# Kernel optimization log

Hardware: AMD Instinct MI355X
Metric: run time of the kernel (lower is better)

The kernel has to match this reference:

```python
import jax, jax.numpy as jnp
import numpy as np

NEG_SLOPE = 0.2
EPS = 1e-16  # PyG softmax denominator epsilon


def gatv2_layer(x, src, dst, W_l, W_r, att, bias, num_nodes, heads, out_dim, concat):
    # x: [N, F_in]; src/dst: [E] (self-loops already included)
    x_l = (x @ W_l).reshape(num_nodes, heads, out_dim)  # source transform
    x_r = (x @ W_r).reshape(num_nodes, heads, out_dim)  # target transform
    # GATv2 scoring: a^T LeakyReLU(x_l[j] + x_r[i])
    e = jax.nn.leaky_relu(x_l[src] + x_r[dst], NEG_SLOPE)       # [E, H, D]
    logits = jnp.einsum('ehd,hd->eh', e, att)                    # [E, H]
    # segment softmax over incoming edges of each target node
    m = jax.ops.segment_max(logits, dst, num_segments=num_nodes)  # [N, H]
    ex = jnp.exp(logits - m[dst])                                 # [E, H]
    denom = jax.ops.segment_sum(ex, dst, num_segments=num_nodes)  # [N, H]
    alpha = ex / (denom[dst] + EPS)                               # [E, H]
    msg = x_l[src] * alpha[:, :, None]                            # [E, H, D]
    out = jax.ops.segment_sum(msg, dst, num_segments=num_nodes)   # [N, H, D]
    if concat:
        out = out.reshape(num_nodes, heads * out_dim)
    else:
        out = out.mean(axis=1)
    return out + bias


def setup_inputs() -> dict:
    key = jax.random.key(0)
    ks = jax.random.split(key, 10)
    N, E, F_in, H, D, F_out = 50000, 400000, 256, 4, 128, 64

    def glorot(k, shape, fan):
        return jax.random.normal(k, shape, dtype=jnp.float32) * (1.0 / np.sqrt(fan))

    return {
        'x': jax.random.normal(ks[0], (N, F_in), dtype=jnp.float32),
        'edge_index': jax.random.randint(ks[1], (2, E), 0, N, dtype=jnp.int64),
        'W_l1': glorot(ks[2], (F_in, H * D), F_in),
        'W_r1': glorot(ks[3], (F_in, H * D), F_in),
        'att1': glorot(ks[4], (H, D), D),
        'b1': jnp.zeros((H * D,), dtype=jnp.float32),
        'W_l2': glorot(ks[5], (H * D, F_out), H * D),
        'W_r2': glorot(ks[6], (H * D, F_out), H * D),
        'att2': glorot(ks[7], (1, F_out), F_out),
        'b2': jnp.zeros((F_out,), dtype=jnp.float32),
    }


def reference(x, edge_index, W_l1, W_r1, att1, b1, W_l2, W_r2, att2, b2):
    N = x.shape[0]
    # add self-loops (PyG GATv2Conv default add_self_loops=True)
    loops = jnp.arange(N, dtype=edge_index.dtype)
    src = jnp.concatenate([edge_index[0], loops])
    dst = jnp.concatenate([edge_index[1], loops])
    # dropout(p=0.6) is identity in eval mode
    h = gatv2_layer(x, src, dst, W_l1, W_r1, att1, b1, N, heads=4, out_dim=128, concat=True)
    h = jax.nn.elu(h)
    out = gatv2_layer(h, src, dst, W_l2, W_r2, att2, b2, N, heads=1, out_dim=64, concat=False)
    return out
```

## Files before the change

kernel.cpp:

```cpp
#include <hip/hip_runtime.h>
#include <hip/hip_bf16.h>
#include <math.h>


#define NEG_SLOPE 0.2f

typedef _Float16 half8 __attribute__((ext_vector_type(8)));
typedef float f32x4 __attribute__((ext_vector_type(4)));

struct __align__(4) h2f { _Float16 x, y; };


__global__ __launch_bounds__(256) void k_zero(int* __restrict__ p, int n) {
    int i = blockIdx.x * 256 + threadIdx.x;
    if (i < n) p[i] = 0;
}

__global__ __launch_bounds__(256) void k_count(const int* __restrict__ ei, int* __restrict__ counts,
                                               int E, int Etot) {
    int i = blockIdx.x * 256 + threadIdx.x;
    if (i >= Etot) return;
    int dst = (i < E) ? ei[E + i] : (i - E);
    atomicAdd(&counts[dst], 1);
}

__global__ __launch_bounds__(1024) void k_scan_a(const int* __restrict__ counts, int* __restrict__ offs,
                                                 int* __restrict__ partial, int n) {
    __shared__ int buf[1024];
    int b = blockIdx.x, t = threadIdx.x;
    int i = b * 1024 + t;
    int v = (i < n) ? counts[i] : 0;
    buf[t] = v;
    __syncthreads();
    #pragma unroll
    for (int off = 1; off < 1024; off <<= 1) {
        int add = (t >= off) ? buf[t - off] : 0;
        __syncthreads();
        buf[t] += add;
        __syncthreads();
    }
    if (i < n) offs[i + 1] = buf[t];
    if (t == 1023) partial[b] = buf[1023];
}

__global__ __launch_bounds__(1024) void k_scan_b(int* __restrict__ partial, int nb) {
    __shared__ int buf[1024];
    int t = threadIdx.x;
    int v = (t < nb) ? partial[t] : 0;
    buf[t] = v;
    __syncthreads();
    #pragma unroll
    for (int off = 1; off < 1024; off <<= 1) {
        int add = (t >= off) ? buf[t - off] : 0;
        __syncthreads();
        buf[t] += add;
        __syncthreads();
    }
    if (t < nb) partial[t] = buf[t] - v;
}

__global__ __launch_bounds__(256) void k_scan_c(int* __restrict__ offs, int* __restrict__ cursor,
                                                const int* __restrict__ partial, int n) {
    int i = blockIdx.x * 256 + threadIdx.x;
    if (i == 0) { offs[0] = 0; cursor[0] = 0; }
    if (i < n) {
        int v = offs[i + 1] + partial[i >> 10];
        offs[i + 1] = v;
        cursor[i + 1] = v;
    }
}

__global__ __launch_bounds__(256) void k_fill(const int* __restrict__ ei, int* __restrict__ cursor,
                                              int* __restrict__ csr_src, int E, int Etot) {
    int i = blockIdx.x * 256 + threadIdx.x;
    if (i >= Etot) return;
    int src, dst;
    if (i < E) { src = ei[i]; dst = ei[E + i]; }
    else       { src = i - E; dst = i - E; }
    int pos = atomicAdd(&cursor[dst], 1);
    csr_src[pos] = src;
}


__global__ __launch_bounds__(256) void k_cast_x(const float* __restrict__ in, _Float16* __restrict__ out,
                                                int n8) {
    int i = blockIdx.x * 256 + threadIdx.x;
    if (i >= n8) return;
    const float4* p = (const float4*)(in + i * 8);
    float4 a = p[0], b = p[1];
    half8 v;
    v[0] = (_Float16)a.x; v[1] = (_Float16)a.y; v[2] = (_Float16)a.z; v[3] = (_Float16)a.w;
    v[4] = (_Float16)b.x; v[5] = (_Float16)b.y; v[6] = (_Float16)b.z; v[7] = (_Float16)b.w;
    *(half8*)(out + i * 8) = v;
}

__global__ __launch_bounds__(256) void k_cast_wcat(const float* __restrict__ Wa, const float* __restrict__ Wb,
                                                   _Float16* __restrict__ out, int K, int Nh) {
    int i = blockIdx.x * 256 + threadIdx.x;
    int total = 2 * Nh * K;
    if (i >= total) return;
    int n = i / K, k = i - n * K;
    float v = (n < Nh) ? Wa[k * Nh + n] : Wb[k * Nh + (n - Nh)];
    out[i] = (_Float16)v;
}


#define LDSPITCH 40

__global__ __launch_bounds__(256) void k_gemm_f16(const _Float16* __restrict__ A,
                                                  const _Float16* __restrict__ Bt,
                                                  _Float16* __restrict__ C,
                                                  int M, int N, int K) {
    __shared__ _Float16 As[128 * LDSPITCH];
    __shared__ _Float16 Bs[128 * LDSPITCH];

    int tid = threadIdx.x;
    int lane = tid & 63;
    int wave = tid >> 6;
    int wm = wave >> 1, wn = wave & 1;
    int l15 = lane & 15, q = lane >> 4;

    int tileM = blockIdx.x * 128;
    int tileN = blockIdx.y * 128;

    int srow = tid >> 2;
    int scg  = (tid & 3) * 8;

    f32x4 acc[4][4];
    #pragma unroll
    for (int i = 0; i < 4; ++i)
        #pragma unroll
        for (int j = 0; j < 4; ++j)
            acc[i][j] = (f32x4)(0.f);

    for (int k0 = 0; k0 < K; k0 += 32) {
        float4 va0, va1, vb0, vb1;
        {
            int r0 = tileM + srow, r1 = tileM + srow + 64;
            const float4 z = make_float4(0.f, 0.f, 0.f, 0.f);
            va0 = (r0 < M) ? *(const float4*)(A + (long)r0 * K + k0 + scg) : z;
            va1 = (r1 < M) ? *(const float4*)(A + (long)r1 * K + k0 + scg) : z;
            vb0 = *(const float4*)(Bt + (long)(tileN + srow) * K + k0 + scg);
            vb1 = *(const float4*)(Bt + (long)(tileN + srow + 64) * K + k0 + scg);
        }
        __syncthreads();
        *(float4*)(As + srow * LDSPITCH + scg) = va0;
        *(float4*)(As + (srow + 64) * LDSPITCH + scg) = va1;
        *(float4*)(Bs + srow * LDSPITCH + scg) = vb0;
        *(float4*)(Bs + (srow + 64) * LDSPITCH + scg) = vb1;
        __syncthreads();

        half8 af[4], bf[4];
        #pragma unroll
        for (int i = 0; i < 4; ++i)
            af[i] = *(half8*)(As + (wm * 64 + i * 16 + l15) * LDSPITCH + q * 8);
        #pragma unroll
        for (int j = 0; j < 4; ++j)
            bf[j] = *(half8*)(Bs + (wn * 64 + j * 16 + l15) * LDSPITCH + q * 8);
        #pragma unroll
        for (int i = 0; i < 4; ++i)
            #pragma unroll
            for (int j = 0; j < 4; ++j)
                acc[i][j] = __builtin_amdgcn_mfma_f32_16x16x32_f16(af[i], bf[j], acc[i][j], 0, 0, 0);
    }

    #pragma unroll
    for (int i = 0; i < 4; ++i) {
        #pragma unroll
        for (int r = 0; r < 4; ++r) {
            int grow = tileM + wm * 64 + i * 16 + q * 4 + r;
            if (grow < M) {
                #pragma unroll
                for (int j = 0; j < 4; ++j) {
                    int gcol = tileN + wn * 64 + j * 16 + l15;
                    C[(long)grow * N + gcol] = (_Float16)acc[i][j][r];
                }
            }
        }
    }
}


__global__ __launch_bounds__(256) void k_attn1(const _Float16* __restrict__ xlr,
                                               const float* __restrict__ att, const float* __restrict__ b1,
                                               const int* __restrict__ offs, const int* __restrict__ csr_src,
                                               _Float16* __restrict__ hout, int N) {
    int wave = threadIdx.x >> 6;
    int lane = threadIdx.x & 63;
    int node = blockIdx.x * 4 + wave;
    if (node >= N) return;

    int cbase = (lane >> 4) * 128 + (lane & 15) * 8;

    half8 xrv = *(const half8*)(xlr + (long)node * 1024 + 512 + cbase);
    float xr[8], at[8];
    #pragma unroll
    for (int j = 0; j < 8; ++j) { xr[j] = (float)xrv[j]; at[j] = att[cbase + j]; }

    float l = 0.f;
    float acc[8] = {};

    int e0 = offs[node], e1 = offs[node + 1];
    int src = csr_src[e0];
    half8 xlv = *(const half8*)(xlr + (long)src * 1024 + cbase);

    for (int e = e0; e < e1; ++e) {
        half8 cur = xlv;
        if (e + 1 < e1) {
            int s2 = csr_src[e + 1];
            xlv = *(const half8*)(xlr + (long)s2 * 1024 + cbase);
        }
        float xf[8];
        float p = 0.f;
        #pragma unroll
        for (int j = 0; j < 8; ++j) {
            xf[j] = (float)cur[j];
            float t = xf[j] + xr[j];
            t = fmaxf(t, NEG_SLOPE * t);
            p = fmaf(t, at[j], p);
        }
        #pragma unroll
        for (int off = 1; off <= 8; off <<= 1) p += __shfl_xor(p, off, 64);
        float w = __expf(p);
        l += w;
        #pragma unroll
        for (int j = 0; j < 8; ++j) acc[j] = fmaf(w, xf[j], acc[j]);
    }

    float inv = 1.f / (l + 1e-16f);
    half8 ov;
    #pragma unroll
    for (int j = 0; j < 8; ++j) {
        float o = fmaf(acc[j], inv, b1[cbase + j]);
        o = (o > 0.f) ? o : (__expf(o) - 1.f);
        ov[j] = (_Float16)o;
    }
    *(half8*)(hout + (long)node * 512 + cbase) = ov;
}


__global__ __launch_bounds__(256) void k_attn2(const _Float16* __restrict__ xlr2,
                                               const float* __restrict__ att, const float* __restrict__ b2,
                                               const int* __restrict__ offs, const int* __restrict__ csr_src,
                                               float* __restrict__ out, int N) {
    int wave = threadIdx.x >> 6;
    int lane = threadIdx.x & 63;
    int node = blockIdx.x * 4 + wave;
    if (node >= N) return;

    float xrv = (float)xlr2[(long)node * 128 + 64 + lane];
    float av  = att[lane];

    float l = 0.f, acc = 0.f;
    int e0 = offs[node], e1 = offs[node + 1];
    int src = csr_src[e0];
    float xlv = (float)xlr2[(long)src * 128 + lane];

    for (int e = e0; e < e1; ++e) {
        float x = xlv;
        if (e + 1 < e1) {
            int s2 = csr_src[e + 1];
            xlv = (float)xlr2[(long)s2 * 128 + lane];
        }
        float t = x + xrv;
        t = fmaxf(t, NEG_SLOPE * t);
        float p = t * av;
        #pragma unroll
        for (int off = 1; off <= 32; off <<= 1) p += __shfl_xor(p, off, 64);
        float w = __expf(p);
        l += w;
        acc = fmaf(w, x, acc);
    }
    out[(long)node * 64 + lane] = acc / (l + 1e-16f) + b2[lane];
}


extern "C" void kernel_launch(void* const* d_in, const int* in_sizes, int n_in,
                              void* d_out, int out_size, void* d_ws, size_t ws_size,
                              hipStream_t stream) {
    const float* x    = (const float*)d_in[0];
    const int*   ei   = (const int*)d_in[1];
    const float* Wl1  = (const float*)d_in[2];
    const float* Wr1  = (const float*)d_in[3];
    const float* att1 = (const float*)d_in[4];
    const float* b1   = (const float*)d_in[5];
    const float* Wl2  = (const float*)d_in[6];
    const float* Wr2  = (const float*)d_in[7];
    const float* att2 = (const float*)d_in[8];
    const float* b2   = (const float*)d_in[9];
    float* out = (float*)d_out;

    const int F_IN = 256;
    int N = in_sizes[0] / F_IN;
    int E = in_sizes[1] / 2;
    int Etot = E + N;
    int nScanBlocks = (N + 1023) / 1024;

    char* p = (char*)d_ws;
    auto carve = [&](size_t bytes) -> void* {
        void* r = (void*)p;
        p += (bytes + 255) & ~(size_t)255;
        return r;
    };
    _Float16* xh   = (_Float16*)carve((size_t)N * 256 * 2);
    _Float16* W1T  = (_Float16*)carve((size_t)1024 * 256 * 2);
    _Float16* W2T  = (_Float16*)carve((size_t)128 * 512 * 2);
    _Float16* C1   = (_Float16*)carve((size_t)N * 1024 * 2);
    _Float16* h    = (_Float16*)carve((size_t)N * 512 * 2);
    _Float16* C2   = (_Float16*)carve((size_t)N * 128 * 2);
    int* counts  = (int*)carve((size_t)N * 4);
    int* offs    = (int*)carve((size_t)(N + 1) * 4);
    int* cursor  = (int*)carve((size_t)(N + 1) * 4);
    int* partial = (int*)carve((size_t)nScanBlocks * 4);
    int* csr     = (int*)carve((size_t)Etot * 4);

    int gN    = (N + 255) / 256;
    int gEtot = (Etot + 255) / 256;

    k_cast_x<<<(N * 256 / 8 + 255) / 256, 256, 0, stream>>>(x, xh, N * 256 / 8);
    k_cast_wcat<<<(1024 * 256 + 255) / 256, 256, 0, stream>>>(Wl1, Wr1, W1T, 256, 512);
    k_cast_wcat<<<(128 * 512 + 255) / 256, 256, 0, stream>>>(Wl2, Wr2, W2T, 512, 64);

    k_zero<<<gN, 256, 0, stream>>>(counts, N);
    k_count<<<gEtot, 256, 0, stream>>>(ei, counts, E, Etot);
    k_scan_a<<<nScanBlocks, 1024, 0, stream>>>(counts, offs, partial, N);
    k_scan_b<<<1, 1024, 0, stream>>>(partial, nScanBlocks);
    k_scan_c<<<gN, 256, 0, stream>>>(offs, cursor, partial, N);
    k_fill<<<gEtot, 256, 0, stream>>>(ei, cursor, csr, E, Etot);

    {
        dim3 grid((N + 127) / 128, 1024 / 128);
        k_gemm_f16<<<grid, 256, 0, stream>>>(xh, W1T, C1, N, 1024, 256);
    }
    k_attn1<<<(N + 3) / 4, 256, 0, stream>>>(C1, att1, b1, offs, csr, h, N);

    {
        dim3 grid((N + 127) / 128, 1);
        k_gemm_f16<<<grid, 256, 0, stream>>>(h, W2T, C2, N, 128, 512);
    }
    k_attn2<<<(N + 3) / 4, 256, 0, stream>>>(C2, att2, b2, offs, csr, out, N);
}
```

Baseline: 389.9 us.

## Use packed fp16 dot2 scoring, deeper index prefetch, fused weight casts, N-major GEMM grid

Layer-1 attention scoring now runs on packed half2 math with an fdot2 accumulate instead of per-element fp32 converts and FMAs. Both attention kernels prefetch the source index two edges ahead so the index load no longer sits on the gather path. The two weight-cast kernels are merged into one launch, the zeroing kernel is replaced with hipMemsetAsync, and the GEMM grid is linearised so the N tiles that share an M tile run back to back. fp16 LeakyReLU and logit accumulation lose some precision compared with fp32.

```diff
diff --git a/kernel.cpp b/kernel.cpp
--- a/kernel.cpp
+++ b/kernel.cpp
@@ -6,15 +6,9 @@
 #define NEG_SLOPE 0.2f
 
 typedef _Float16 half8 __attribute__((ext_vector_type(8)));
+typedef _Float16 h2 __attribute__((ext_vector_type(2)));
 typedef float f32x4 __attribute__((ext_vector_type(4)));
 
-struct __align__(4) h2f { _Float16 x, y; };
-
-
-__global__ __launch_bounds__(256) void k_zero(int* __restrict__ p, int n) {
-    int i = blockIdx.x * 256 + threadIdx.x;
-    if (i < n) p[i] = 0;
-}
 
 __global__ __launch_bounds__(256) void k_count(const int* __restrict__ ei, int* __restrict__ counts,
                                                int E, int Etot) {
@@ -94,14 +88,22 @@
     *(half8*)(out + i * 8) = v;
 }
 
-__global__ __launch_bounds__(256) void k_cast_wcat(const float* __restrict__ Wa, const float* __restrict__ Wb,
-                                                   _Float16* __restrict__ out, int K, int Nh) {
-    int i = blockIdx.x * 256 + threadIdx.x;
-    int total = 2 * Nh * K;
-    if (i >= total) return;
-    int n = i / K, k = i - n * K;
-    float v = (n < Nh) ? Wa[k * Nh + n] : Wb[k * Nh + (n - Nh)];
-    out[i] = (_Float16)v;
+__global__ __launch_bounds__(256) void k_cast_w(const float* __restrict__ Wl1, const float* __restrict__ Wr1,
+                                                const float* __restrict__ Wl2, const float* __restrict__ Wr2,
+                                                _Float16* __restrict__ W1T, _Float16* __restrict__ W2T) {
+    int i = blockIdx.x * 256 + threadIdx.x;
+    const int T1 = 1024 * 256;
+    const int T2 = 128 * 512;
+    if (i < T1) {
+        int n = i >> 8, k = i & 255;
+        float v = (n < 512) ? Wl1[k * 512 + n] : Wr1[k * 512 + (n - 512)];
+        W1T[i] = (_Float16)v;
+    } else if (i < T1 + T2) {
+        int j = i - T1;
+        int n = j >> 9, k = j & 511;
+        float v = (n < 64) ? Wl2[k * 64 + n] : Wr2[k * 64 + (n - 64)];
+        W2T[j] = (_Float16)v;
+    }
 }
 
 
@@ -110,7 +112,7 @@
 __global__ __launch_bounds__(256) void k_gemm_f16(const _Float16* __restrict__ A,
                                                   const _Float16* __restrict__ Bt,
                                                   _Float16* __restrict__ C,
-                                                  int M, int N, int K) {
+                                                  int M, int N, int K, int ntiles) {
     __shared__ _Float16 As[128 * LDSPITCH];
     __shared__ _Float16 Bs[128 * LDSPITCH];
 
@@ -120,8 +122,10 @@
     int wm = wave >> 1, wn = wave & 1;
     int l15 = lane & 15, q = lane >> 4;
 
-    int tileM = blockIdx.x * 128;
-    int tileN = blockIdx.y * 128;
+    int ntile = blockIdx.x % ntiles;
+    int mtile = blockIdx.x / ntiles;
+    int tileM = mtile * 128;
+    int tileN = ntile * 128;
 
     int srow = tid >> 2;
     int scg  = (tid & 3) * 8;
@@ -181,6 +185,14 @@
 }
 
 
+__device__ __forceinline__ float dot2acc(h2 a, h2 b, float c) {
+#if __has_builtin(__builtin_amdgcn_fdot2)
+    return __builtin_amdgcn_fdot2(a, b, c, false);
+#else
+    return fmaf((float)a[1], (float)b[1], fmaf((float)a[0], (float)b[0], c));
+#endif
+}
+
 __global__ __launch_bounds__(256) void k_attn1(const _Float16* __restrict__ xlr,
                                                const float* __restrict__ att, const float* __restrict__ b1,
                                                const int* __restrict__ offs, const int* __restrict__ csr_src,
@@ -192,39 +204,50 @@
 
     int cbase = (lane >> 4) * 128 + (lane & 15) * 8;
 
-    half8 xrv = *(const half8*)(xlr + (long)node * 1024 + 512 + cbase);
-    float xr[8], at[8];
-    #pragma unroll
-    for (int j = 0; j < 8; ++j) { xr[j] = (float)xrv[j]; at[j] = att[cbase + j]; }
+    half8 xrv8 = *(const half8*)(xlr + (long)node * 1024 + 512 + cbase);
+    h2 xr[4], at[4];
+    #pragma unroll
+    for (int j = 0; j < 4; ++j) {
+        xr[j][0] = xrv8[2 * j]; xr[j][1] = xrv8[2 * j + 1];
+        at[j][0] = (_Float16)att[cbase + 2 * j];
+        at[j][1] = (_Float16)att[cbase + 2 * j + 1];
+    }
+    const h2 ns2 = {(_Float16)NEG_SLOPE, (_Float16)NEG_SLOPE};
 
     float l = 0.f;
     float acc[8] = {};
 
     int e0 = offs[node], e1 = offs[node + 1];
-    int src = csr_src[e0];
-    half8 xlv = *(const half8*)(xlr + (long)src * 1024 + cbase);
+    int s_next = csr_src[e0];
+    int s_next2 = (e0 + 1 < e1) ? csr_src[e0 + 1] : 0;
+    half8 xlv = *(const half8*)(xlr + (long)s_next * 1024 + cbase);
 
     for (int e = e0; e < e1; ++e) {
         half8 cur = xlv;
-        if (e + 1 < e1) {
-            int s2 = csr_src[e + 1];
-            xlv = *(const half8*)(xlr + (long)s2 * 1024 + cbase);
-        }
-        float xf[8];
+        int s_pf = s_next2;
+        if (e + 2 < e1) s_next2 = csr_src[e + 2];
+        if (e + 1 < e1) xlv = *(const half8*)(xlr + (long)s_pf * 1024 + cbase);
+
+        const h2* cp = (const h2*)&cur;
         float p = 0.f;
         #pragma unroll
-        for (int j = 0; j < 8; ++j) {
-            xf[j] = (float)cur[j];
-            float t = xf[j] + xr[j];
-            t = fmaxf(t, NEG_SLOPE * t);
-            p = fmaf(t, at[j], p);
+        for (int j = 0; j < 4; ++j) {
+            h2 t = cp[j] + xr[j];
+#if __has_builtin(__builtin_elementwise_max)
+            t = __builtin_elementwise_max(t, t * ns2);
+#else
+            h2 tn = t * ns2;
+            t[0] = (t[0] > tn[0]) ? t[0] : tn[0];
+            t[1] = (t[1] > tn[1]) ? t[1] : tn[1];
+#endif
+            p = dot2acc(t, at[j], p);
         }
         #pragma unroll
         for (int off = 1; off <= 8; off <<= 1) p += __shfl_xor(p, off, 64);
         float w = __expf(p);
         l += w;
         #pragma unroll
-        for (int j = 0; j < 8; ++j) acc[j] = fmaf(w, xf[j], acc[j]);
+        for (int j = 0; j < 8; ++j) acc[j] = fmaf(w, (float)cur[j], acc[j]);
     }
 
     float inv = 1.f / (l + 1e-16f);
@@ -253,15 +276,16 @@
 
     float l = 0.f, acc = 0.f;
     int e0 = offs[node], e1 = offs[node + 1];
-    int src = csr_src[e0];
-    float xlv = (float)xlr2[(long)src * 128 + lane];
+    int s_next = csr_src[e0];
+    int s_next2 = (e0 + 1 < e1) ? csr_src[e0 + 1] : 0;
+    float xlv = (float)xlr2[(long)s_next * 128 + lane];
 
     for (int e = e0; e < e1; ++e) {
         float x = xlv;
-        if (e + 1 < e1) {
-            int s2 = csr_src[e + 1];
-            xlv = (float)xlr2[(long)s2 * 128 + lane];
-        }
+        int s_pf = s_next2;
+        if (e + 2 < e1) s_next2 = csr_src[e + 2];
+        if (e + 1 < e1) xlv = (float)xlr2[(long)s_pf * 128 + lane];
+
         float t = x + xrv;
         t = fmaxf(t, NEG_SLOPE * t);
         float p = t * av;
@@ -318,10 +342,12 @@
     int gEtot = (Etot + 255) / 256;
 
     k_cast_x<<<(N * 256 / 8 + 255) / 256, 256, 0, stream>>>(x, xh, N * 256 / 8);
-    k_cast_wcat<<<(1024 * 256 + 255) / 256, 256, 0, stream>>>(Wl1, Wr1, W1T, 256, 512);
-    k_cast_wcat<<<(128 * 512 + 255) / 256, 256, 0, stream>>>(Wl2, Wr2, W2T, 512, 64);
-
-    k_zero<<<gN, 256, 0, stream>>>(counts, N);
+    {
+        int total = 1024 * 256 + 128 * 512;
+        k_cast_w<<<(total + 255) / 256, 256, 0, stream>>>(Wl1, Wr1, Wl2, Wr2, W1T, W2T);
+    }
+
+    hipMemsetAsync(counts, 0, (size_t)N * 4, stream);
     k_count<<<gEtot, 256, 0, stream>>>(ei, counts, E, Etot);
     k_scan_a<<<nScanBlocks, 1024, 0, stream>>>(counts, offs, partial, N);
     k_scan_b<<<1, 1024, 0, stream>>>(partial, nScanBlocks);
@@ -329,14 +355,14 @@
     k_fill<<<gEtot, 256, 0, stream>>>(ei, cursor, csr, E, Etot);
 
     {
-        dim3 grid((N + 127) / 128, 1024 / 128);
-        k_gemm_f16<<<grid, 256, 0, stream>>>(xh, W1T, C1, N, 1024, 256);
+        int mtiles = (N + 127) / 128, ntiles = 1024 / 128;
+        k_gemm_f16<<<mtiles * ntiles, 256, 0, stream>>>(xh, W1T, C1, N, 1024, 256, ntiles);
     }
     k_attn1<<<(N + 3) / 4, 256, 0, stream>>>(C1, att1, b1, offs, csr, h, N);
 
     {
-        dim3 grid((N + 127) / 128, 1);
-        k_gemm_f16<<<grid, 256, 0, stream>>>(h, W2T, C2, N, 128, 512);
+        int mtiles = (N + 127) / 128;
+        k_gemm_f16<<<mtiles, 256, 0, stream>>>(h, W2T, C2, N, 128, 512, 1);
     }
     k_attn2<<<(N + 3) / 4, 256, 0, stream>>>(C2, att2, b2, offs, csr, out, N);
 }
```

New measurement: 372.8 us. 4.4% less time.
